# Kernel tuning notes

Measured on AMD Instinct MI355X. Metric: run time of the kernel, lower is better.

The kernel has to match this reference:

```python
import jax, jax.numpy as jnp
import numpy as np
from jax import lax

SCORE_THRESH = 0.05
NMS_THRESH = 0.5
DET_PER_IMG = 100
K_PRE = 2048  # pre-NMS candidate cap (batched_nms is never run on N*C dense candidates)
BBOX_XFORM_CLIP = float(np.log(1000.0 / 16.0))
WX, WY, WW, WH = 10.0, 10.0, 5.0, 5.0


def _decode(reg, props):
    # reg: [N, C, 4] deltas, props: [N, 4] xyxy -> [N, C, 4] xyxy (torchvision BoxCoder.decode)
    w = props[:, 2] - props[:, 0]
    h = props[:, 3] - props[:, 1]
    cx = props[:, 0] + 0.5 * w
    cy = props[:, 1] + 0.5 * h
    dx = reg[..., 0] / WX
    dy = reg[..., 1] / WY
    dw = jnp.minimum(reg[..., 2] / WW, BBOX_XFORM_CLIP)
    dh = jnp.minimum(reg[..., 3] / WH, BBOX_XFORM_CLIP)
    pcx = dx * w[:, None] + cx[:, None]
    pcy = dy * h[:, None] + cy[:, None]
    pw = jnp.exp(dw) * w[:, None]
    ph = jnp.exp(dh) * h[:, None]
    return jnp.stack([pcx - 0.5 * pw, pcy - 0.5 * ph, pcx + 0.5 * pw, pcy + 0.5 * ph], axis=-1)


def _pairwise_iou(b):
    # b: [K, 4] -> [K, K]
    area = (b[:, 2] - b[:, 0]) * (b[:, 3] - b[:, 1])
    lt = jnp.maximum(b[:, None, :2], b[None, :, :2])
    rb = jnp.minimum(b[:, None, 2:], b[None, :, 2:])
    wh = jnp.clip(rb - lt, 0.0)
    inter = wh[..., 0] * wh[..., 1]
    return inter / (area[:, None] + area[None, :] - inter)


def _greedy_nms(iou, valid, thresh):
    # boxes assumed sorted by descending score; valid: [K] bool initial keep mask
    K = iou.shape[0]
    idx = jnp.arange(K)
    def body(i, keep):
        sup = (iou[i] > thresh) & (idx > i) & keep[i]
        return keep & (~sup)
    return lax.fori_loop(0, K, body, valid)


def _process_image(logits, reg, props, img_h, img_w):
    # logits: [N, C], reg: [N, 4C], props: [N, 4]
    N, C = logits.shape
    scores = jax.nn.softmax(logits, axis=-1)[:, 1:]          # [N, C-1] drop background
    boxes = _decode(reg.reshape(N, C, 4), props)[:, 1:]      # [N, C-1, 4]
    boxes = jnp.stack([
        jnp.clip(boxes[..., 0], 0.0, img_w),
        jnp.clip(boxes[..., 1], 0.0, img_h),
        jnp.clip(boxes[..., 2], 0.0, img_w),
        jnp.clip(boxes[..., 3], 0.0, img_h),
    ], axis=-1)
    labels = jnp.broadcast_to(jnp.arange(1, C), (N, C - 1))
    boxes = boxes.reshape(-1, 4)       # [M, 4], M = N*(C-1)
    scores = scores.reshape(-1)
    labels = labels.reshape(-1)
    wd = boxes[:, 2] - boxes[:, 0]
    ht = boxes[:, 3] - boxes[:, 1]
    valid = (scores > SCORE_THRESH) & (wd >= 1.0) & (ht >= 1.0)  # score thresh + remove_small_boxes
    masked = jnp.where(valid, scores, -1.0)
    top_s, top_i = lax.top_k(masked, K_PRE)
    tb = boxes[top_i]
    tl = labels[top_i]
    tvalid = top_s > SCORE_THRESH
    # batched_nms via per-class coordinate offsets
    off = tl.astype(tb.dtype) * (jnp.max(tb) + 1.0)
    keep = _greedy_nms(_pairwise_iou(tb + off[:, None]), tvalid, NMS_THRESH)
    ks = jnp.where(keep, top_s, -1.0)
    fs, fi = lax.top_k(ks, DET_PER_IMG)
    fvalid = fs > SCORE_THRESH
    out_boxes = jnp.where(fvalid[:, None], tb[fi], 0.0)
    out_scores = jnp.where(fvalid, fs, 0.0)
    out_labels = jnp.where(fvalid, tl[fi], -1)
    return out_boxes, out_scores, out_labels


def setup_inputs() -> dict:
    key = jax.random.key(0)
    k1, k2, k3 = jax.random.split(key, 3)
    B, N, C, H, W = 8, 4000, 91, 800, 800
    pts = jax.random.uniform(k1, (B, N, 2, 2), dtype=jnp.float32, minval=0.0, maxval=float(W))
    proposals = jnp.concatenate([pts.min(axis=2), pts.max(axis=2)], axis=-1)  # valid xyxy
    class_logits = jax.random.normal(k2, (B * N, C), dtype=jnp.float32)
    box_regression = 0.5 * jax.random.normal(k3, (B * N, 4 * C), dtype=jnp.float32)
    return {"class_logits": class_logits, "box_regression": box_regression,
            "proposals": proposals, "img_h": H, "img_w": W}


def reference(class_logits, box_regression, proposals, img_h, img_w):
    B, N, _ = proposals.shape
    C = class_logits.shape[-1]
    logits = class_logits.reshape(B, N, C)
    reg = box_regression.reshape(B, N, 4 * C)
    fn = lambda l, r, p: _process_image(l, r, p, float(img_h), float(img_w))
    boxes, scores, labels = jax.vmap(fn)(logits, reg, proposals)
    return boxes, scores, labels
```

## Files before the change

### kernel.cpp

```cpp
#include <hip/hip_runtime.h>
#include <stdint.h>

typedef unsigned int u32;
typedef unsigned long long u64;
typedef __attribute__((ext_vector_type(2))) unsigned long long u64x2;

#define BIMG 8
#define NPROP 4000
#define NCLS 91
#define CM1 90
#define MCAND (NPROP * CM1)
#define KPRE 2048
#define NBUCKET 4096
#define NREP 8
#define SELCAP 16384
#define NSLOT 32
#define DETS 100
#define WLCAP 2048
#define SCORE_T 0.05f
#define NMS_T 0.5f
#define BBOX_CLIP 4.135166556742356f

#define HISTREP_OFF ((size_t)0)
#define BCNTREP_OFF (HISTREP_OFF + (size_t)NREP * BIMG * NBUCKET * 4)
#define META_OFF    (BCNTREP_OFF + (size_t)NREP * BIMG * NBUCKET * 4)
#define ZERO_BYTES  (META_OFF + 4096)
#define START_OFF   (ZERO_BYTES)
#define HISTTOT_OFF (START_OFF + (size_t)BIMG * NBUCKET * 4)
#define STARTREP_OFF (HISTTOT_OFF + (size_t)BIMG * NBUCKET * 4)
#define SEL_OFF     (STARTREP_OFF + (size_t)NREP * BIMG * NBUCKET * 4)
#define TBOX_OFF    (SEL_OFF + (size_t)BIMG * SELCAP * 8)
#define TSB_OFF     (TBOX_OFF + (size_t)BIMG * KPRE * 16)
#define TSC_OFF     (TSB_OFF + (size_t)BIMG * KPRE * 16)
#define TLB_OFF     (TSC_OFF + (size_t)BIMG * KPRE * 4)
#define TVLB_OFF    (TLB_OFF + (size_t)BIMG * KPRE * 4)
#define WLIST_OFF   (TVLB_OFF + (size_t)BIMG * 32 * 8)
#define CLIST_OFF   (WLIST_OFF + (size_t)BIMG * WLCAP * 4)
#define CVALID_OFF  (CLIST_OFF + (size_t)BIMG * NPROP * NSLOT * 8)
#define MASK_OFF    (CVALID_OFF + (size_t)BIMG * NPROP * 2 * 8)
#define WS_NEED     (MASK_OFF + (size_t)BIMG * KPRE * 32 * 8)

__device__ __forceinline__ void decode_clip(const float4 rg, const float w, const float h,
                                            const float cx, const float cy,
                                            const float fw, const float fh, float bx[4]) {
    float dx = rg.x / 10.0f;
    float dy = rg.y / 10.0f;
    float dw = fminf(rg.z / 5.0f, BBOX_CLIP);
    float dh = fminf(rg.w / 5.0f, BBOX_CLIP);
    float pcx = dx * w + cx;
    float pcy = dy * h + cy;
    float pw  = expf(dw) * w;
    float phh = expf(dh) * h;
    bx[0] = fminf(fmaxf(pcx - 0.5f * pw,  0.0f), fw);
    bx[1] = fminf(fmaxf(pcy - 0.5f * phh, 0.0f), fh);
    bx[2] = fminf(fmaxf(pcx + 0.5f * pw,  0.0f), fw);
    bx[3] = fminf(fmaxf(pcy + 0.5f * phh, 0.0f), fh);
}

__global__ __launch_bounds__(256) void k1_score_hist(
    const float* __restrict__ logits, const float* __restrict__ reg,
    const float* __restrict__ props, const int* __restrict__ imh, const int* __restrict__ imw,
    u32* __restrict__ histrep, u64* __restrict__ clist, u64* __restrict__ cvalid) {
    const int lane = threadIdx.x & 63;
    const int pid = blockIdx.x * 4 + (threadIdx.x >> 6);
    if (pid >= BIMG * NPROP) return;
    const int img = pid / NPROP;
    const float fw = (float)imw[0], fh = (float)imh[0];
    const float* lrow = logits + (size_t)pid * NCLS;
    float v0 = lrow[lane];
    float v1 = (lane < 27) ? lrow[lane + 64] : -3.0e38f;
    float mx = fmaxf(v0, v1);
#pragma unroll
    for (int o = 32; o > 0; o >>= 1) mx = fmaxf(mx, __shfl_xor(mx, o));
    float es = expf(v0 - mx) + ((lane < 27) ? expf(v1 - mx) : 0.0f);
#pragma unroll
    for (int o = 32; o > 0; o >>= 1) es += __shfl_xor(es, o);
    const float thr = mx + logf(es) - 2.9967323f;
    float4 p = reinterpret_cast<const float4*>(props)[pid];
    const float w = p.z - p.x, h = p.w - p.y;
    const float cx = p.x + 0.5f * w, cy = p.y + 0.5f * h;
    const float4* rrow = reinterpret_cast<const float4*>(reg) + (size_t)pid * NCLS;
    const int n = pid - img * NPROP;
    const int rep = n & (NREP - 1);
    const float sh0 = __shfl(v0, (lane + 1) & 63);
    const float sh1 = __shfl(v1, (lane + 1) & 63);
    u64 w0 = 0ull, w1 = 0ull;
    u32 base1 = 0;
#pragma unroll
    for (int batch = 0; batch < 2; ++batch) {
        const int ci = lane + batch * 64;
        bool valid = false;
        u32 ob = 0u;
        if (ci < CM1) {
            const float l = (batch == 0) ? ((lane == 63) ? sh1 : sh0) : sh1;
            if (l > thr) {
                float sc = expf(l - mx) / es;
                float4 rg = rrow[ci + 1];
                float bx[4];
                decode_clip(rg, w, h, cx, cy, fw, fh, bx);
                valid = (sc > SCORE_T) && (bx[2] - bx[0] >= 1.0f) && (bx[3] - bx[1] >= 1.0f);
                if (valid) {
                    ob = __float_as_uint(sc) | 0x80000000u;
                    atomicAdd(&histrep[((size_t)rep * BIMG + img) * NBUCKET + (ob >> 20)], 1u);
                }
            }
        }
        const u64 bal = __ballot(valid);
        if (batch == 0) { w0 = bal; base1 = (u32)__popcll(bal); }
        else            { w1 = bal; }
        if (valid) {
            const u32 pre = (u32)__popcll(bal & ((1ull << lane) - 1ull));
            const u32 slot = (batch == 0) ? pre : (base1 + pre);
            const u32 idx = (u32)n * CM1 + (u32)ci;
            clist[(size_t)pid * NSLOT + slot] = ((u64)ob << 32) | (u32)(~idx);
        }
    }
    if (lane == 0) {
        u64x2 v; v.x = w0; v.y = w1;
        reinterpret_cast<u64x2*>(cvalid)[pid] = v;
    }
}

__global__ __launch_bounds__(256) void k2_scan(
    const u32* __restrict__ histrep, u32* __restrict__ histtot,
    u32* __restrict__ start, u32* __restrict__ startrep, u32* __restrict__ meta,
    u32* __restrict__ wlist) {
    const int img = blockIdx.x;
    const int td = threadIdx.x;
    const int lane = td & 63, wv = td >> 6;
    u32 cnt[16]; u32 tsum = 0;
#pragma unroll
    for (int k = 0; k < 16; ++k) {
        const int bk = NBUCKET - 1 - (td * 16 + k);
        u32 c = 0;
#pragma unroll
        for (int r = 0; r < NREP; ++r)
            c += histrep[((size_t)r * BIMG + img) * NBUCKET + bk];
        cnt[k] = c; tsum += c;
    }
    u32 inc = tsum;
#pragma unroll
    for (int o = 1; o < 64; o <<= 1) { u32 t = __shfl_up(inc, o); if (lane >= o) inc += t; }
    __shared__ u32 wsum[4];
    __shared__ u32 TbkS, Vs;
    if (td == 0) TbkS = 0u;
    if (lane == 63) wsum[wv] = inc;
    __syncthreads();
    u32 wbase = 0;
    for (int i = 0; i < wv; ++i) wbase += wsum[i];
    if (td == 255) Vs = wbase + inc;
    const u32 excl0 = wbase + inc - tsum;
    u32 excl = excl0;
#pragma unroll
    for (int k = 0; k < 16; ++k) {
        const int bk = NBUCKET - 1 - (td * 16 + k);
        const u32 c = cnt[k];
        start[img * NBUCKET + bk] = excl;
        histtot[img * NBUCKET + bk] = c;
        u32 sub = excl;
#pragma unroll
        for (int r = 0; r < NREP; ++r) {
            startrep[((size_t)r * BIMG + img) * NBUCKET + bk] = sub;
            sub += histrep[((size_t)r * BIMG + img) * NBUCKET + bk];
        }
        if (c > 0 && excl < KPRE && excl + c >= KPRE) TbkS = (u32)bk;
        excl += c;
    }
    u32 qcnt = 0;
    {
        u32 e = excl0;
#pragma unroll
        for (int k = 0; k < 16; ++k) { if (cnt[k] >= 2 && e < KPRE) ++qcnt; e += cnt[k]; }
    }
    u32 qinc = qcnt;
#pragma unroll
    for (int o = 1; o < 64; o <<= 1) { u32 t = __shfl_up(qinc, o); if (lane >= o) qinc += t; }
    __shared__ u32 qws[4];
    if (lane == 63) qws[wv] = qinc;
    __syncthreads();
    u32 qbase = 0;
    for (int i = 0; i < wv; ++i) qbase += qws[i];
    u32 qoff = qbase + qinc - qcnt;
    {
        u32 e = excl0;
#pragma unroll
        for (int k = 0; k < 16; ++k) {
            const int bk = NBUCKET - 1 - (td * 16 + k);
            if (cnt[k] >= 2 && e < KPRE && qoff < WLCAP) wlist[img * WLCAP + (qoff++)] = (u32)bk;
            e += cnt[k];
        }
    }
    if (td == 255) meta[img * 8 + 3] = qbase + qinc;
    __syncthreads();
    if (td == 0) {
        u32 V = Vs;
        meta[img * 8 + 0] = V;
        meta[img * 8 + 1] = TbkS;
        meta[img * 8 + 2] = (V < KPRE) ? (KPRE - V) : 0u;
    }
}

__global__ __launch_bounds__(256) void k3_compact(
    const u64* __restrict__ clist, const u64* __restrict__ cvalid,
    const u32* __restrict__ startrep, const u32* __restrict__ meta,
    u32* __restrict__ bcntrep, u64* __restrict__ sel) {
    const u32 t = blockIdx.x * 256 + threadIdx.x;
    const u32 row = t >> 5;
    const u32 slot = t & 31;
    if (row < (u32)(BIMG * NPROP)) {
        const u64x2 vb = reinterpret_cast<const u64x2*>(cvalid)[row];
        const u32 rcnt = (u32)__popcll(vb.x) + (u32)__popcll(vb.y);
        if (slot < rcnt) {
            const u32 img = row / NPROP;
            const u32 n = row - img * NPROP;
            const u32 rep = n & (NREP - 1);
            const u64 e = clist[(size_t)row * NSLOT + slot];
            const u32 bk = (u32)(e >> 52);
            if (bk >= meta[img * 8 + 1]) {
                const size_t ri = ((size_t)rep * BIMG + img) * NBUCKET + bk;
                const u32 pos = startrep[ri] + atomicAdd(&bcntrep[ri], 1u);
                if (pos < SELCAP) sel[(size_t)img * SELCAP + pos] = e;
            }
        }
    }
    if (blockIdx.x < BIMG && threadIdx.x < 64) {
        const int img = blockIdx.x;
        const u32 need = meta[img * 8 + 2];
        if (need != 0) {
            const u32 V = meta[img * 8 + 0];
            const int lv = threadIdx.x;
            const u32 ORDN1 = 0x407FFFFFu;
            u32 filled = 0;
            for (u32 b0 = 0; b0 < MCAND && filled < need; b0 += 64) {
                const u32 idx = b0 + (u32)lv;
                bool inv = false;
                if (idx < MCAND) {
                    const u32 nn = (u32)(((u64)idx * 3054198967ull) >> 38);
                    const u32 cq = idx - nn * 90u;
                    const u64 wb = cvalid[((size_t)img * NPROP + nn) * 2 + (cq >> 6)];
                    inv = ((wb >> (cq & 63)) & 1ull) == 0ull;
                }
                const u64 bal = __ballot(inv);
                const u32 pre = (u32)__popcll(bal & ((1ull << lv) - 1ull));
                if (inv && (filled + pre) < need)
                    sel[(size_t)img * SELCAP + V + filled + pre] =
                        ((u64)ORDN1 << 32) | (u32)(~idx);
                filled += (u32)__popcll(bal);
            }
        }
    }
}

__global__ __launch_bounds__(256) void k4_sortseg(
    const u32* __restrict__ histtot, const u32* __restrict__ start,
    const u32* __restrict__ meta, const u32* __restrict__ wlist, u64* __restrict__ sel) {
    __shared__ u64 arr[4096];
    const int img = blockIdx.y;
    const int tid = threadIdx.x;
    const u32 wcount = meta[img * 8 + 3];
    for (u32 wi = blockIdx.x; wi < wcount; wi += gridDim.x) {
        const u32 bk = (wi < WLCAP) ? wlist[img * WLCAP + wi] : 0u;
        u32 cnt = histtot[img * NBUCKET + bk];
        u32 st = start[img * NBUCKET + bk];
        if (cnt <= 64 || st >= KPRE) continue;
        if (st + cnt > SELCAP) cnt = SELCAP - st;
        if (cnt > 4096) cnt = 4096;
        int n = 1;
        while (n < (int)cnt) n <<= 1;
        u64* seg = sel + (size_t)img * SELCAP + st;
        for (int i = tid; i < n; i += 256) arr[i] = (i < (int)cnt) ? seg[i] : 0ull;
        __syncthreads();
        for (int k = 2; k <= n; k <<= 1)
            for (int j = k >> 1; j > 0; j >>= 1) {
                for (int i = tid; i < n; i += 256) {
                    int ixj = i ^ j;
                    if (ixj > i) {
                        u64 a = arr[i], b = arr[ixj];
                        bool swp = ((i & k) == 0) ? (a < b) : (a > b);
                        if (swp) { arr[i] = b; arr[ixj] = a; }
                    }
                }
                __syncthreads();
            }
        for (int i = tid; i < (int)cnt; i += 256) seg[i] = arr[i];
        __syncthreads();
    }
    const int wv = tid >> 6, lane = tid & 63;
    for (u32 wi = blockIdx.x * 4 + wv; wi < wcount; wi += gridDim.x * 4) {
        const u32 bk = (wi < WLCAP) ? wlist[img * WLCAP + wi] : 0u;
        u32 cnt = histtot[img * NBUCKET + bk];
        u32 st = start[img * NBUCKET + bk];
        if (cnt < 2 || cnt > 64 || st >= KPRE) continue;
        if (st + cnt > SELCAP) cnt = SELCAP - st;
        u64* seg = sel + (size_t)img * SELCAP + st;
        u64 key = (lane < (int)cnt) ? seg[lane] : 0ull;
#pragma unroll
        for (int k = 2; k <= 64; k <<= 1) {
#pragma unroll
            for (int j = k >> 1; j > 0; j >>= 1) {
                u64 other = __shfl_xor(key, j);
                bool takeMax = ((lane & j) == 0) == ((lane & k) == 0);
                u64 hi2 = (key > other) ? key : other;
                u64 lo2 = (key > other) ? other : key;
                key = takeMax ? hi2 : lo2;
            }
        }
        if (lane < (int)cnt) seg[lane] = key;
    }
}

__global__ __launch_bounds__(256) void k5_gather(
    const u64* __restrict__ sel, const float* __restrict__ reg, const float* __restrict__ props,
    const int* __restrict__ imh, const int* __restrict__ imw,
    float* __restrict__ tbox, float* __restrict__ tsb, float* __restrict__ tsc,
    int* __restrict__ tlb, u64* __restrict__ tvlb) {
    const int img = blockIdx.x;
    const int tid = threadIdx.x;
    const float fw = (float)imw[0], fh = (float)imh[0];
    float bx[8][4];
    int lab[8];
    float lm = -3.0e38f;
#pragma unroll
    for (int t = 0; t < 8; ++t) {
        int s = t * 256 + tid;
        u64 key = sel[(size_t)img * SELCAP + s];
        u32 o = (u32)(key >> 32);
        u32 idx = ~((u32)key);
        u32 b = (o & 0x80000000u) ? (o & 0x7FFFFFFFu) : ~o;
        float sc = __uint_as_float(b);
        u32 n = idx / CM1;
        int c = (int)(idx - n * CM1) + 1;
        int pid = img * NPROP + (int)n;
        float4 p = reinterpret_cast<const float4*>(props)[pid];
        float w = p.z - p.x, h = p.w - p.y;
        float cx = p.x + 0.5f * w, cy = p.y + 0.5f * h;
        float4 rg = reinterpret_cast<const float4*>(reg)[(size_t)pid * NCLS + c];
        decode_clip(rg, w, h, cx, cy, fw, fh, bx[t]);
        lab[t] = c;
        lm = fmaxf(lm, fmaxf(fmaxf(bx[t][0], bx[t][1]), fmaxf(bx[t][2], bx[t][3])));
        reinterpret_cast<float4*>(tbox)[(size_t)img * KPRE + s] =
            make_float4(bx[t][0], bx[t][1], bx[t][2], bx[t][3]);
        tsc[(size_t)img * KPRE + s] = sc;
        tlb[(size_t)img * KPRE + s] = c;
        u64 bw = __ballot(sc > SCORE_T);
        if ((tid & 63) == 0) tvlb[img * 32 + t * 4 + (tid >> 6)] = bw;
    }
#pragma unroll
    for (int o2 = 32; o2 > 0; o2 >>= 1) lm = fmaxf(lm, __shfl_xor(lm, o2));
    __shared__ float wm[4];
    if ((tid & 63) == 0) wm[tid >> 6] = lm;
    __syncthreads();
    float mplus = fmaxf(fmaxf(wm[0], wm[1]), fmaxf(wm[2], wm[3])) + 1.0f;
#pragma unroll
    for (int t = 0; t < 8; ++t) {
        int s = t * 256 + tid;
        float off = (float)lab[t] * mplus;
        reinterpret_cast<float4*>(tsb)[(size_t)img * KPRE + s] =
            make_float4(bx[t][0] + off, bx[t][1] + off, bx[t][2] + off, bx[t][3] + off);
    }
}

__global__ __launch_bounds__(64) void k6_mask(
    const float* __restrict__ tsb, u64* __restrict__ mask) {
    const int img = blockIdx.z;
    const int tid = threadIdx.x;
    if (blockIdx.x < blockIdx.y) {
        const int i = blockIdx.y * 64 + tid;
        mask[((size_t)img * KPRE + i) * 32 + blockIdx.x] = 0ull;
        return;
    }
    const int j0 = blockIdx.x * 64;
    const int i0 = blockIdx.y * 64;
    __shared__ float4 cb[64];
    __shared__ float ca[64];
    float4 c = reinterpret_cast<const float4*>(tsb)[(size_t)img * KPRE + j0 + tid];
    cb[tid] = c;
    ca[tid] = (c.z - c.x) * (c.w - c.y);
    __syncthreads();
    const int i = i0 + tid;
    float4 r = reinterpret_cast<const float4*>(tsb)[(size_t)img * KPRE + i];
    float ra = (r.z - r.x) * (r.w - r.y);
    u64 bits = 0ull;
#pragma unroll 8
    for (int jj = 0; jj < 64; ++jj) {
        int j = j0 + jj;
        float4 cc = cb[jj];
        float wv = fmaxf(fminf(r.z, cc.z) - fmaxf(r.x, cc.x), 0.0f);
        float hv = fmaxf(fminf(r.w, cc.w) - fmaxf(r.y, cc.y), 0.0f);
        float inter = wv * hv;
        float iou = inter / ((ra + ca[jj]) - inter);
        if ((iou > NMS_T) && (j > i)) bits |= (1ull << jj);
    }
    mask[((size_t)img * KPRE + i) * 32 + (j0 >> 6)] = bits;
}

__device__ __forceinline__ u64 rdlane64(u64 v, int l) {
    u32 lo = (u32)__builtin_amdgcn_readlane((int)(u32)v, l);
    u32 hi = (u32)__builtin_amdgcn_readlane((int)(u32)(v >> 32), l);
    return ((u64)hi << 32) | lo;
}

__device__ __forceinline__ void g2l16(const void* g, void* l) {
    __builtin_amdgcn_global_load_lds(
        (const __attribute__((address_space(1))) void*)g,
        (__attribute__((address_space(3))) void*)l, 16, 0, 0);
}

__global__ __launch_bounds__(64) void k7_nms_sel(
    const u64* __restrict__ mask, const u64* __restrict__ tvlb,
    const float* __restrict__ tsc, const float* __restrict__ tbox,
    const int* __restrict__ tlb, float* __restrict__ out) {
    __shared__ u64 smem[4096];
    const int img = blockIdx.x;
    const int lane = threadIdx.x;
    const int lg = lane >> 4;
    const u64* mrow = mask + (size_t)img * KPRE * 32;

    u64 accx, accy, rp;
    {
        u64 nv = 0ull;
        if (lane < 32) nv = ~tvlb[img * 32 + lane];
        rp   = __shfl(nv, 0);
        accx = __shfl(nv, (lane & 15) * 2);
        accy = __shfl(nv, (lane & 15) * 2 + 1);
    }

    {
        const char* gsrc = (const char*)mrow + (size_t)lane * 16;
#pragma unroll
        for (int t = 0; t < 16; ++t)
            g2l16(gsrc + (size_t)t * 1024, (char*)smem + (size_t)t * 1024);
    }
    u64 diag = mrow[(size_t)lane * 32];

    u32 tk = 0;
    int bcut = 31;

#pragma unroll 1
    for (int b = 0; b < 32; ++b) {
        const size_t base32 = (size_t)b * 2048;
        const u64* cbuf = smem + (size_t)(b & 1) * 2048;

        u64 diagn = 0ull;
        if (b + 1 < 32) {
            diagn = mrow[base32 + 2048 + (size_t)lane * 32 + (b + 1)];
            const char* gsrc = (const char*)(mrow + base32 + 2048) + (size_t)lane * 16;
            char* nb_l = (char*)(smem + (size_t)((b + 1) & 1) * 2048);
#pragma unroll
            for (int t = 0; t < 16; ++t)
                g2l16(gsrc + (size_t)t * 1024, nb_l + (size_t)t * 1024);
        }

        u64 A = rp;
#pragma unroll
        for (int u = 0; u < 64; ++u) {
            u64 row = rdlane64(diag, u);
            if (!((A >> u) & 1ull)) A |= row;
        }
        const u64 keptw = ~A;

        if (b + 1 < 32) asm volatile("s_waitcnt vmcnt(17)" ::: "memory");
        else            asm volatile("s_waitcnt vmcnt(0)" ::: "memory");

#define LDV(K) u64x2 v##K = *(const u64x2*)&cbuf[128 * (K) + 2 * lane];
#define PRV(K) { u32 nib = (u32)(keptw >> (4 * (K))) & 15u; \
                 u32 kb = (nib >> lg) & 1u; \
                 accx |= kb ? v##K.x : 0ull; accy |= kb ? v##K.y : 0ull; }
        LDV(0) LDV(1) LDV(2) LDV(3)
        LDV(4) LDV(5) LDV(6) LDV(7)     PRV(0) PRV(1) PRV(2) PRV(3)
        LDV(8) LDV(9) LDV(10) LDV(11)   PRV(4) PRV(5) PRV(6) PRV(7)
        LDV(12) LDV(13) LDV(14) LDV(15) PRV(8) PRV(9) PRV(10) PRV(11)
        PRV(12) PRV(13) PRV(14) PRV(15)
#undef LDV
#undef PRV

        tk += (u32)__popcll(keptw);
        if (tk >= (u32)DETS) { bcut = b; break; }

        const int nb2 = b + 1;
        if (nb2 < 32) {
            u64 asel = (nb2 & 1) ? accy : accx;
            const int sl = (nb2 >> 1) & 15;
            rp = rdlane64(asel, sl) | rdlane64(asel, sl + 16) |
                 rdlane64(asel, sl + 32) | rdlane64(asel, sl + 48);
        }
        diag = diagn;
    }

    asm volatile("s_waitcnt vmcnt(0)" ::: "memory");

    accx |= __shfl_xor(accx, 16); accx |= __shfl_xor(accx, 32);
    accy |= __shfl_xor(accy, 16); accy |= __shfl_xor(accy, 32);

    u64 mxv = __shfl(accx, (lane >> 1) & 15);
    u64 myv = __shfl(accy, (lane >> 1) & 15);
    u64 kw = (lane & 1) ? ~myv : ~mxv;
    if (lane >= 32 || lane > bcut) kw = 0ull;

    u32 cnt = (u32)__popcll(kw);
    u32 inc = cnt;
#pragma unroll
    for (int o = 1; o < 64; o <<= 1) { u32 t = __shfl_up(inc, o); if (lane >= o) inc += t; }
    const u32 excl = inc - cnt;
    const u32 total = (u32)__shfl(inc, 63);

    float* ob0 = out + (size_t)img * DETS * 4;
    float* os0 = out + (size_t)BIMG * DETS * 4 + (size_t)img * DETS;
    float* ol0 = out + (size_t)BIMG * DETS * 5 + (size_t)img * DETS;

#pragma unroll
    for (int t = 0; t < 2; ++t) {
        u32 r = (u32)lane + (u32)t * 64;
        if (r < DETS && r >= total) {
            reinterpret_cast<float4*>(ob0)[r] = make_float4(0.f, 0.f, 0.f, 0.f);
            os0[r] = 0.0f;
            ol0[r] = -1.0f;
        }
    }
    u64 w = kw;
    u32 r = excl;
    while (w != 0ull && r < DETS) {
        int p = __ffsll((unsigned long long)w) - 1;
        w &= (w - 1ull);
        u32 s = (u32)lane * 64u + (u32)p;
        reinterpret_cast<float4*>(ob0)[r] =
            reinterpret_cast<const float4*>(tbox)[(size_t)img * KPRE + s];
        os0[r] = tsc[(size_t)img * KPRE + s];
        ol0[r] = (float)tlb[(size_t)img * KPRE + s];
        ++r;
    }
}

extern "C" void kernel_launch(void* const* d_in, const int* in_sizes, int n_in,
                              void* d_out, int out_size, void* d_ws, size_t ws_size,
                              hipStream_t stream) {
    const float* logits = (const float*)d_in[0];
    const float* reg    = (const float*)d_in[1];
    const float* props  = (const float*)d_in[2];
    const int*   imh    = (const int*)d_in[3];
    const int*   imw    = (const int*)d_in[4];
    float* out = (float*)d_out;
    char* ws = (char*)d_ws;
    if (ws_size < WS_NEED) return;

    u32* histrep  = (u32*)(ws + HISTREP_OFF);
    u32* bcntrep  = (u32*)(ws + BCNTREP_OFF);
    u32* meta     = (u32*)(ws + META_OFF);
    u32* start    = (u32*)(ws + START_OFF);
    u32* histtot  = (u32*)(ws + HISTTOT_OFF);
    u32* startrep = (u32*)(ws + STARTREP_OFF);
    u64* sel  = (u64*)(ws + SEL_OFF);
    float* tbox = (float*)(ws + TBOX_OFF);
    float* tsb  = (float*)(ws + TSB_OFF);
    float* tsc  = (float*)(ws + TSC_OFF);
    int*   tlb  = (int*)(ws + TLB_OFF);
    u64*   tvlb = (u64*)(ws + TVLB_OFF);
    u32*   wlist = (u32*)(ws + WLIST_OFF);
    u64*   clist = (u64*)(ws + CLIST_OFF);
    u64*   cvalid = (u64*)(ws + CVALID_OFF);
    u64*   mask = (u64*)(ws + MASK_OFF);

    hipMemsetAsync(d_ws, 0, ZERO_BYTES, stream);

    k1_score_hist<<<BIMG * NPROP / 4, 256, 0, stream>>>(logits, reg, props, imh, imw,
                                                        histrep, clist, cvalid);
    k2_scan<<<BIMG, 256, 0, stream>>>(histrep, histtot, start, startrep, meta, wlist);
    k3_compact<<<(BIMG * NPROP * NSLOT) / 256, 256, 0, stream>>>(clist, cvalid, startrep,
                                                                 meta, bcntrep, sel);
    k4_sortseg<<<dim3(64, BIMG), 256, 0, stream>>>(histtot, start, meta, wlist, sel);
    k5_gather<<<BIMG, 256, 0, stream>>>(sel, reg, props, imh, imw, tbox, tsb, tsc, tlb, tvlb);
    k6_mask<<<dim3(32, 32, BIMG), 64, 0, stream>>>(tsb, mask);
    k7_nms_sel<<<BIMG, 64, 0, stream>>>(mask, tvlb, tsc, tbox, tlb, out);
}
```

Baseline: 261.6 us.

## Stage histograms in LDS, shrink compact grid, widen gather, triangular mask grid

Several independent changes. The per-replica histogram layout is transposed so k2_scan can stage a whole image's histograms into padded shared memory, and startrep is stored rep-contiguous. k3_compact now launches 4 threads per row that loop over slots instead of 32 threads per row. k5_gather runs 1024 threads per image instead of 256, and k6_mask launches only the 528 upper-triangular tiles. Because the zero-fill of lower-triangle mask tiles is dropped, k7 instead masks the loaded words by column range so unwritten tiles are ignored.

```diff
diff --git a/kernel.cpp b/kernel.cpp
--- a/kernel.cpp
+++ b/kernel.cpp
@@ -101,7 +101,7 @@
                 valid = (sc > SCORE_T) && (bx[2] - bx[0] >= 1.0f) && (bx[3] - bx[1] >= 1.0f);
                 if (valid) {
                     ob = __float_as_uint(sc) | 0x80000000u;
-                    atomicAdd(&histrep[((size_t)rep * BIMG + img) * NBUCKET + (ob >> 20)], 1u);
+                    atomicAdd(&histrep[((size_t)img * NREP + rep) * NBUCKET + (ob >> 20)], 1u);
                 }
             }
         }
@@ -125,17 +125,29 @@
     const u32* __restrict__ histrep, u32* __restrict__ histtot,
     u32* __restrict__ start, u32* __restrict__ startrep, u32* __restrict__ meta,
     u32* __restrict__ wlist) {
+    __shared__ u32 hs[NREP * 4352];
     const int img = blockIdx.x;
     const int td = threadIdx.x;
     const int lane = td & 63, wv = td >> 6;
+    {
+        const u32* hg = histrep + (size_t)img * NREP * NBUCKET;
+        for (int i = td; i < (NREP * NBUCKET) / 4; i += 256) {
+            uint4 v = reinterpret_cast<const uint4*>(hg)[i];
+            const int r = i >> 10;
+            const int b0 = (i * 4) & 4095;
+            u32* dst = &hs[r * 4352 + b0 + (b0 >> 4)];
+            dst[0] = v.x; dst[1] = v.y; dst[2] = v.z; dst[3] = v.w;
+        }
+    }
+    __syncthreads();
+#define HREAD(r, bk) hs[(r) * 4352 + (bk) + ((bk) >> 4)]
     u32 cnt[16]; u32 tsum = 0;
 #pragma unroll
     for (int k = 0; k < 16; ++k) {
         const int bk = NBUCKET - 1 - (td * 16 + k);
         u32 c = 0;
 #pragma unroll
-        for (int r = 0; r < NREP; ++r)
-            c += histrep[((size_t)r * BIMG + img) * NBUCKET + bk];
+        for (int r = 0; r < NREP; ++r) c += HREAD(r, bk);
         cnt[k] = c; tsum += c;
     }
     u32 inc = tsum;
@@ -160,12 +172,13 @@
         u32 sub = excl;
 #pragma unroll
         for (int r = 0; r < NREP; ++r) {
-            startrep[((size_t)r * BIMG + img) * NBUCKET + bk] = sub;
-            sub += histrep[((size_t)r * BIMG + img) * NBUCKET + bk];
+            startrep[((size_t)img * NBUCKET + bk) * NREP + r] = sub;
+            sub += HREAD(r, bk);
         }
         if (c > 0 && excl < KPRE && excl + c >= KPRE) TbkS = (u32)bk;
         excl += c;
     }
+#undef HREAD
     u32 qcnt = 0;
     {
         u32 e = excl0;
@@ -205,21 +218,24 @@
     const u32* __restrict__ startrep, const u32* __restrict__ meta,
     u32* __restrict__ bcntrep, u64* __restrict__ sel) {
     const u32 t = blockIdx.x * 256 + threadIdx.x;
-    const u32 row = t >> 5;
-    const u32 slot = t & 31;
+    const u32 row = t >> 2;
+    const u32 s0 = t & 3;
     if (row < (u32)(BIMG * NPROP)) {
         const u64x2 vb = reinterpret_cast<const u64x2*>(cvalid)[row];
         const u32 rcnt = (u32)__popcll(vb.x) + (u32)__popcll(vb.y);
-        if (slot < rcnt) {
+        if (s0 < rcnt) {
             const u32 img = row / NPROP;
             const u32 n = row - img * NPROP;
             const u32 rep = n & (NREP - 1);
-            const u64 e = clist[(size_t)row * NSLOT + slot];
-            const u32 bk = (u32)(e >> 52);
-            if (bk >= meta[img * 8 + 1]) {
-                const size_t ri = ((size_t)rep * BIMG + img) * NBUCKET + bk;
-                const u32 pos = startrep[ri] + atomicAdd(&bcntrep[ri], 1u);
-                if (pos < SELCAP) sel[(size_t)img * SELCAP + pos] = e;
+            const u32 cutoff = meta[img * 8 + 1];
+            for (u32 slot = s0; slot < rcnt; slot += 4) {
+                const u64 e = clist[(size_t)row * NSLOT + slot];
+                const u32 bk = (u32)(e >> 52);
+                if (bk >= cutoff) {
+                    const u32 pos = startrep[((size_t)img * NBUCKET + bk) * NREP + rep] +
+                        atomicAdd(&bcntrep[((size_t)rep * BIMG + img) * NBUCKET + bk], 1u);
+                    if (pos < SELCAP) sel[(size_t)img * SELCAP + pos] = e;
+                }
             }
         }
     }
@@ -309,7 +325,7 @@
     }
 }
 
-__global__ __launch_bounds__(256) void k5_gather(
+__global__ __launch_bounds__(1024) void k5_gather(
     const u64* __restrict__ sel, const float* __restrict__ reg, const float* __restrict__ props,
     const int* __restrict__ imh, const int* __restrict__ imw,
     float* __restrict__ tbox, float* __restrict__ tsb, float* __restrict__ tsc,
@@ -317,12 +333,12 @@
     const int img = blockIdx.x;
     const int tid = threadIdx.x;
     const float fw = (float)imw[0], fh = (float)imh[0];
-    float bx[8][4];
-    int lab[8];
+    float bx[2][4];
+    int lab[2];
     float lm = -3.0e38f;
 #pragma unroll
-    for (int t = 0; t < 8; ++t) {
-        int s = t * 256 + tid;
+    for (int t = 0; t < 2; ++t) {
+        int s = t * 1024 + tid;
         u64 key = sel[(size_t)img * SELCAP + s];
         u32 o = (u32)(key >> 32);
         u32 idx = ~((u32)key);
@@ -343,17 +359,20 @@
         tsc[(size_t)img * KPRE + s] = sc;
         tlb[(size_t)img * KPRE + s] = c;
         u64 bw = __ballot(sc > SCORE_T);
-        if ((tid & 63) == 0) tvlb[img * 32 + t * 4 + (tid >> 6)] = bw;
+        if ((tid & 63) == 0) tvlb[img * 32 + t * 16 + (tid >> 6)] = bw;
     }
 #pragma unroll
     for (int o2 = 32; o2 > 0; o2 >>= 1) lm = fmaxf(lm, __shfl_xor(lm, o2));
-    __shared__ float wm[4];
+    __shared__ float wm[16];
     if ((tid & 63) == 0) wm[tid >> 6] = lm;
     __syncthreads();
-    float mplus = fmaxf(fmaxf(wm[0], wm[1]), fmaxf(wm[2], wm[3])) + 1.0f;
-#pragma unroll
-    for (int t = 0; t < 8; ++t) {
-        int s = t * 256 + tid;
+    float m = wm[0];
+#pragma unroll
+    for (int i = 1; i < 16; ++i) m = fmaxf(m, wm[i]);
+    const float mplus = m + 1.0f;
+#pragma unroll
+    for (int t = 0; t < 2; ++t) {
+        int s = t * 1024 + tid;
         float off = (float)lab[t] * mplus;
         reinterpret_cast<float4*>(tsb)[(size_t)img * KPRE + s] =
             make_float4(bx[t][0] + off, bx[t][1] + off, bx[t][2] + off, bx[t][3] + off);
@@ -362,15 +381,16 @@
 
 __global__ __launch_bounds__(64) void k6_mask(
     const float* __restrict__ tsb, u64* __restrict__ mask) {
-    const int img = blockIdx.z;
+    const int img = blockIdx.y;
+    const u32 t = blockIdx.x;
+    float f = sqrtf(8.0f * (float)t + 1.0f);
+    u32 x = (u32)((f - 1.0f) * 0.5f);
+    while ((x + 1) * (x + 2) / 2 <= t) ++x;
+    while (x * (x + 1) / 2 > t) --x;
+    const u32 y = t - x * (x + 1) / 2;
+    const int j0 = (int)x * 64;
+    const int i0 = (int)y * 64;
     const int tid = threadIdx.x;
-    if (blockIdx.x < blockIdx.y) {
-        const int i = blockIdx.y * 64 + tid;
-        mask[((size_t)img * KPRE + i) * 32 + blockIdx.x] = 0ull;
-        return;
-    }
-    const int j0 = blockIdx.x * 64;
-    const int i0 = blockIdx.y * 64;
     __shared__ float4 cb[64];
     __shared__ float ca[64];
     float4 c = reinterpret_cast<const float4*>(tsb)[(size_t)img * KPRE + j0 + tid];
@@ -414,6 +434,7 @@
     const int img = blockIdx.x;
     const int lane = threadIdx.x;
     const int lg = lane >> 4;
+    const int wlo = 2 * (lane & 15);
     const u64* mrow = mask + (size_t)img * KPRE * 32;
 
     u64 accx, accy, rp;
@@ -462,10 +483,13 @@
         if (b + 1 < 32) asm volatile("s_waitcnt vmcnt(17)" ::: "memory");
         else            asm volatile("s_waitcnt vmcnt(0)" ::: "memory");
 
+        const u64 gx = (wlo >= b) ? ~0ull : 0ull;
+        const u64 gy = (wlo + 1 >= b) ? ~0ull : 0ull;
+
 #define LDV(K) u64x2 v##K = *(const u64x2*)&cbuf[128 * (K) + 2 * lane];
 #define PRV(K) { u32 nib = (u32)(keptw >> (4 * (K))) & 15u; \
                  u32 kb = (nib >> lg) & 1u; \
-                 accx |= kb ? v##K.x : 0ull; accy |= kb ? v##K.y : 0ull; }
+                 accx |= kb ? (v##K.x & gx) : 0ull; accy |= kb ? (v##K.y & gy) : 0ull; }
         LDV(0) LDV(1) LDV(2) LDV(3)
         LDV(4) LDV(5) LDV(6) LDV(7)     PRV(0) PRV(1) PRV(2) PRV(3)
         LDV(8) LDV(9) LDV(10) LDV(11)   PRV(4) PRV(5) PRV(6) PRV(7)
@@ -565,10 +589,10 @@
     k1_score_hist<<<BIMG * NPROP / 4, 256, 0, stream>>>(logits, reg, props, imh, imw,
                                                         histrep, clist, cvalid);
     k2_scan<<<BIMG, 256, 0, stream>>>(histrep, histtot, start, startrep, meta, wlist);
-    k3_compact<<<(BIMG * NPROP * NSLOT) / 256, 256, 0, stream>>>(clist, cvalid, startrep,
-                                                                 meta, bcntrep, sel);
+    k3_compact<<<(BIMG * NPROP * 4) / 256, 256, 0, stream>>>(clist, cvalid, startrep,
+                                                             meta, bcntrep, sel);
     k4_sortseg<<<dim3(64, BIMG), 256, 0, stream>>>(histtot, start, meta, wlist, sel);
-    k5_gather<<<BIMG, 256, 0, stream>>>(sel, reg, props, imh, imw, tbox, tsb, tsc, tlb, tvlb);
-    k6_mask<<<dim3(32, 32, BIMG), 64, 0, stream>>>(tsb, mask);
+    k5_gather<<<BIMG, 1024, 0, stream>>>(sel, reg, props, imh, imw, tbox, tsb, tsc, tlb, tvlb);
+    k6_mask<<<dim3(528, BIMG), 64, 0, stream>>>(tsb, mask);
     k7_nms_sel<<<BIMG, 64, 0, stream>>>(mask, tvlb, tsc, tbox, tlb, out);
 }
```

Result: faster. 229.7 us (-12.2%).
